# Optimization experiments

Hardware: AMD Instinct MI355X
Metric: run time of the kernel (lower is better)

The kernel has to match this reference:

```python
import jax, jax.numpy as jnp
import numpy as np

MODEL_DIM = 256
HIST = 8
HID = 512
N_NEURONS = 64
IN_DIM = MODEL_DIM * (1 + HIST)  # 2304
BATCH = 32
FMIN, FMAX = 0.5, 40.0
TICK_INTERVAL = 0.1
LN_EPS = 1e-5


def setup_inputs() -> dict:
    key = jax.random.key(0)
    ks = jax.random.split(key, 8)
    def lin(k, shape, fan_in):
        return (jax.random.normal(k, shape, jnp.float32) / np.sqrt(fan_in)).astype(jnp.float32)
    return {
        "input_embedding": jax.random.normal(ks[0], (BATCH, MODEL_DIM), jnp.float32),
        "pre_activations": jax.random.normal(ks[1], (HIST, MODEL_DIM), jnp.float32),
        "Wp": lin(ks[2], (MODEL_DIM, MODEL_DIM), MODEL_DIM),
        "bp": jnp.zeros((MODEL_DIM,), jnp.float32),
        "W1": lin(ks[3], (N_NEURONS, IN_DIM, HID), IN_DIM),
        "b1": jnp.zeros((N_NEURONS, HID), jnp.float32),
        "W2": lin(ks[4], (N_NEURONS, HID, HID), HID),
        "b2": jnp.zeros((N_NEURONS, HID), jnp.float32),
        "W3": lin(ks[5], (N_NEURONS, HID, MODEL_DIM), HID),
        "b3": jnp.zeros((N_NEURONS, MODEL_DIM), jnp.float32),
        "gamma": jnp.ones((N_NEURONS, MODEL_DIM), jnp.float32),
        "beta": jnp.zeros((N_NEURONS, MODEL_DIM), jnp.float32),
        "tick": 7,
    }


def reference(input_embedding, pre_activations, Wp, bp, W1, b1, W2, b2, W3, b3, gamma, beta, tick):
    B = input_embedding.shape[0]
    # input projection, shared history broadcast across batch
    proj = input_embedding @ Wp + bp                               # (B, D)
    hist = jnp.broadcast_to(pre_activations.reshape(-1)[None, :], (B, HIST * MODEL_DIM))
    x = jnp.concatenate([proj, hist], axis=-1)                     # (B, IN_DIM)
    # all neurons' 3-layer MLPs as batched GEMMs (dropout in eval mode = identity)
    h = jax.nn.gelu(jnp.einsum('bi,nih->bnh', x, W1) + b1, approximate=False)
    h = jax.nn.gelu(jnp.einsum('bnh,nhg->bng', h, W2) + b2, approximate=False)
    y = jnp.einsum('bnh,nhd->bnd', h, W3) + b3                     # (B, N, D)
    # per-neuron LayerNorm over last dim
    mu = jnp.mean(y, axis=-1, keepdims=True)
    var = jnp.mean((y - mu) ** 2, axis=-1, keepdims=True)
    y = (y - mu) * jax.lax.rsqrt(var + LN_EPS) * gamma + beta
    # oscillator modulation: log-spaced freq, deterministic phase
    i = jnp.arange(N_NEURONS, dtype=jnp.float32)
    freq = FMIN * (FMAX / FMIN) ** (i / (N_NEURONS - 1))
    phase = jnp.mod(i * 2.3571, 2.0 * np.pi)
    t = tick * TICK_INTERVAL
    mod = 1.0 + 0.5 * jnp.sin(2.0 * np.pi * freq * t + phase)      # (N,)
    return y * mod[None, :, None]                                  # (B, N, D)
```

## Files before the change

### kernel.cpp

```cpp
#include <hip/hip_runtime.h>
#include <hip/hip_bf16.h>

#define MODEL_DIM 256
#define HIST 8
#define HID 512
#define NNEUR 64
#define IN_DIM 2304
#define BATCH 32

__device__ __forceinline__ float geluf(float x) {
    return 0.5f * x * (1.0f + erff(x * 0.70710678118654752440f));
}
__device__ __forceinline__ float f4c(const float4& v, int j) {
    switch (j) { case 0: return v.x; case 1: return v.y; case 2: return v.z; default: return v.w; }
}

__global__ __launch_bounds__(256) void k_build_x(
        const float* __restrict__ emb, const float* __restrict__ pre,
        const float* __restrict__ Wp, const float* __restrict__ bp,
        float* __restrict__ proj) {
    const int b = blockIdx.x;
    const int d = threadIdx.x;

    __shared__ float e[MODEL_DIM];
    e[d] = emb[b * MODEL_DIM + d];
    __syncthreads();

    float acc = bp[d];
    #pragma unroll 4
    for (int k = 0; k < MODEL_DIM; ++k)
        acc = fmaf(e[k], Wp[(size_t)k * MODEL_DIM + d], acc);
    proj[b * MODEL_DIM + d] = acc;
}

__global__ __launch_bounds__(256, 4) void k_layer1(
        const float* __restrict__ pre, const float* __restrict__ proj,
        const float* __restrict__ W1,
        float* __restrict__ ph, float* __restrict__ pp) {
    __shared__ float lds[2048];
    const int bid = blockIdx.x;
    const int t = threadIdx.x;

    if (bid < 512) {
        const int n  = bid >> 3;
        const int ks = bid & 7;
        const int c4 = t & 127;
        const int kh = t >> 7;
        const int k0 = ks * 256;

        float* ps = lds;
        ps[t] = pre[k0 + t];
        __syncthreads();

        const float* W = W1 + (size_t)n * IN_DIM * HID
                            + (size_t)(MODEL_DIM + k0 + kh * 128) * HID + c4 * 4;
        float4 a = make_float4(0.f, 0.f, 0.f, 0.f);
        const float* psk = ps + kh * 128;
        #pragma unroll 8
        for (int kk = 0; kk < 128; ++kk) {
            float4 w = *((const float4*)(W + (size_t)kk * HID));
            float s = psk[kk];
            a.x = fmaf(s, w.x, a.x);
            a.y = fmaf(s, w.y, a.y);
            a.z = fmaf(s, w.z, a.z);
            a.w = fmaf(s, w.w, a.w);
        }
        float4* red = (float4*)(lds + 256);
        if (kh == 1) red[c4] = a;
        __syncthreads();
        if (kh == 0) {
            float4 b4 = red[c4];
            a.x += b4.x; a.y += b4.y; a.z += b4.z; a.w += b4.w;
            *((float4*)(ph + ((size_t)ks * NNEUR + n) * HID + c4 * 4)) = a;
        }
    } else {
        const int pb = bid - 512;
        const int n  = pb >> 3;
        const int ct = (pb >> 2) & 1;
        const int ks = pb & 3;
        const int cg = t & 63;
        const int rg = t >> 6;
        const int col0 = ct * 256 + cg * 4;
        const int row0 = rg * 8;
        const int k0 = ks * 64;

        float (*xs)[64] = (float(*)[64])lds;
        #pragma unroll
        for (int q = 0; q < 2; ++q) {
            int fi  = t + 256 * q;
            int row = fi >> 4;
            int c4  = fi & 15;
            *((float4*)&xs[row][c4 * 4]) =
                *((const float4*)(proj + (size_t)row * MODEL_DIM + k0 + c4 * 4));
        }
        __syncthreads();

        const float* W = W1 + (size_t)n * IN_DIM * HID + (size_t)k0 * HID + col0;

        float acc[8][4];
        #pragma unroll
        for (int i = 0; i < 8; ++i)
            #pragma unroll
            for (int j = 0; j < 4; ++j) acc[i][j] = 0.0f;

        for (int kg = 0; kg < 64; kg += 4) {
            float4 xv[8];
            #pragma unroll
            for (int i = 0; i < 8; ++i)
                xv[i] = *((const float4*)&xs[row0 + i][kg]);
            #pragma unroll
            for (int j = 0; j < 4; ++j) {
                float4 w = *((const float4*)(W + (size_t)(kg + j) * HID));
                #pragma unroll
                for (int i = 0; i < 8; ++i) {
                    float xvv = f4c(xv[i], j);
                    acc[i][0] = fmaf(xvv, w.x, acc[i][0]);
                    acc[i][1] = fmaf(xvv, w.y, acc[i][1]);
                    acc[i][2] = fmaf(xvv, w.z, acc[i][2]);
                    acc[i][3] = fmaf(xvv, w.w, acc[i][3]);
                }
            }
        }
        float* P = pp + (size_t)(ks * NNEUR + n) * BATCH * HID;
        #pragma unroll
        for (int i = 0; i < 8; ++i)
            *((float4*)(P + (size_t)(row0 + i) * HID + col0)) =
                make_float4(acc[i][0], acc[i][1], acc[i][2], acc[i][3]);
    }
}

__global__ __launch_bounds__(256, 4) void k_layer2(
        const float* __restrict__ pp, const float* __restrict__ ph,
        const float* __restrict__ b1,
        const float* __restrict__ W2, float* __restrict__ p2) {
    const int bid = blockIdx.x;
    const int n  = bid >> 4;
    const int ct = (bid >> 3) & 1;
    const int ks = bid & 7;
    const int t  = threadIdx.x;
    const int cg = t & 63;
    const int rg = t >> 6;
    const int col0 = ct * 256 + cg * 4;
    const int row0 = rg * 8;
    const int k0 = ks * 64;

    const size_t slp = (size_t)NNEUR * BATCH * HID;
    const size_t slh = (size_t)NNEUR * HID;

    __shared__ float xs[BATCH][64];
    #pragma unroll
    for (int q = 0; q < 2; ++q) {
        int fi  = t + 256 * q;
        int row = fi >> 4;
        int c4  = fi & 15;
        const float* a = pp + ((size_t)n * BATCH + row) * HID + k0 + c4 * 4;
        float4 s0 = *((const float4*)(a));
        float4 s1 = *((const float4*)(a + slp));
        float4 s2 = *((const float4*)(a + 2 * slp));
        float4 s3 = *((const float4*)(a + 3 * slp));
        const float* h = ph + (size_t)n * HID + k0 + c4 * 4;
        float4 h0 = *((const float4*)(h));
        float4 h1 = *((const float4*)(h + slh));
        float4 h2 = *((const float4*)(h + 2 * slh));
        float4 h3 = *((const float4*)(h + 3 * slh));
        float4 h4 = *((const float4*)(h + 4 * slh));
        float4 h5 = *((const float4*)(h + 5 * slh));
        float4 h6 = *((const float4*)(h + 6 * slh));
        float4 h7 = *((const float4*)(h + 7 * slh));
        float4 bb = *((const float4*)(b1 + (size_t)n * HID + k0 + c4 * 4));
        *((float4*)&xs[row][c4 * 4]) = make_float4(
            geluf(s0.x+s1.x+s2.x+s3.x + h0.x+h1.x+h2.x+h3.x+h4.x+h5.x+h6.x+h7.x + bb.x),
            geluf(s0.y+s1.y+s2.y+s3.y + h0.y+h1.y+h2.y+h3.y+h4.y+h5.y+h6.y+h7.y + bb.y),
            geluf(s0.z+s1.z+s2.z+s3.z + h0.z+h1.z+h2.z+h3.z+h4.z+h5.z+h6.z+h7.z + bb.z),
            geluf(s0.w+s1.w+s2.w+s3.w + h0.w+h1.w+h2.w+h3.w+h4.w+h5.w+h6.w+h7.w + bb.w));
    }
    __syncthreads();

    const float* W = W2 + (size_t)n * HID * HID + (size_t)k0 * HID + col0;

    float acc[8][4];
    #pragma unroll
    for (int i = 0; i < 8; ++i)
        #pragma unroll
        for (int j = 0; j < 4; ++j) acc[i][j] = 0.0f;

    for (int kg = 0; kg < 64; kg += 4) {
        float4 xv[8];
        #pragma unroll
        for (int i = 0; i < 8; ++i)
            xv[i] = *((const float4*)&xs[row0 + i][kg]);
        #pragma unroll
        for (int j = 0; j < 4; ++j) {
            float4 w = *((const float4*)(W + (size_t)(kg + j) * HID));
            #pragma unroll
            for (int i = 0; i < 8; ++i) {
                float xvv = f4c(xv[i], j);
                acc[i][0] = fmaf(xvv, w.x, acc[i][0]);
                acc[i][1] = fmaf(xvv, w.y, acc[i][1]);
                acc[i][2] = fmaf(xvv, w.z, acc[i][2]);
                acc[i][3] = fmaf(xvv, w.w, acc[i][3]);
            }
        }
    }
    float* P = p2 + (size_t)(ks * NNEUR + n) * BATCH * HID;
    #pragma unroll
    for (int i = 0; i < 8; ++i)
        *((float4*)(P + (size_t)(row0 + i) * HID + col0)) =
            make_float4(acc[i][0], acc[i][1], acc[i][2], acc[i][3]);
}

__global__ __launch_bounds__(256, 4) void k_layer3(
        const float* __restrict__ p2, const float* __restrict__ b2,
        const float* __restrict__ W3, float* __restrict__ p3) {
    const int bid = blockIdx.x;
    const int n  = bid >> 4;
    const int ks = bid & 15;
    const int t  = threadIdx.x;
    const int cg = t & 63;
    const int rg = t >> 6;
    const int col0 = cg * 4;
    const int row0 = rg * 8;
    const int k0 = ks * 32;

    const size_t sl = (size_t)NNEUR * BATCH * HID;

    __shared__ float xs[BATCH][32];
    {
        int row = t >> 3;
        int c4  = t & 7;
        const float* a = p2 + ((size_t)n * BATCH + row) * HID + k0 + c4 * 4;
        float4 s0 = *((const float4*)(a));
        float4 s1 = *((const float4*)(a + sl));
        float4 s2 = *((const float4*)(a + 2 * sl));
        float4 s3 = *((const float4*)(a + 3 * sl));
        float4 s4 = *((const float4*)(a + 4 * sl));
        float4 s5 = *((const float4*)(a + 5 * sl));
        float4 s6 = *((const float4*)(a + 6 * sl));
        float4 s7 = *((const float4*)(a + 7 * sl));
        float4 bb = *((const float4*)(b2 + (size_t)n * HID + k0 + c4 * 4));
        *((float4*)&xs[row][c4 * 4]) = make_float4(
            geluf(s0.x+s1.x+s2.x+s3.x+s4.x+s5.x+s6.x+s7.x + bb.x),
            geluf(s0.y+s1.y+s2.y+s3.y+s4.y+s5.y+s6.y+s7.y + bb.y),
            geluf(s0.z+s1.z+s2.z+s3.z+s4.z+s5.z+s6.z+s7.z + bb.z),
            geluf(s0.w+s1.w+s2.w+s3.w+s4.w+s5.w+s6.w+s7.w + bb.w));
    }
    __syncthreads();

    const float* W = W3 + (size_t)n * HID * MODEL_DIM + (size_t)k0 * MODEL_DIM + col0;

    float acc[8][4];
    #pragma unroll
    for (int i = 0; i < 8; ++i)
        #pragma unroll
        for (int j = 0; j < 4; ++j) acc[i][j] = 0.0f;

    for (int kg = 0; kg < 32; kg += 4) {
        float4 xv[8];
        #pragma unroll
        for (int i = 0; i < 8; ++i)
            xv[i] = *((const float4*)&xs[row0 + i][kg]);
        #pragma unroll
        for (int j = 0; j < 4; ++j) {
            float4 w = *((const float4*)(W + (size_t)(kg + j) * MODEL_DIM));
            #pragma unroll
            for (int i = 0; i < 8; ++i) {
                float xvv = f4c(xv[i], j);
                acc[i][0] = fmaf(xvv, w.x, acc[i][0]);
                acc[i][1] = fmaf(xvv, w.y, acc[i][1]);
                acc[i][2] = fmaf(xvv, w.z, acc[i][2]);
                acc[i][3] = fmaf(xvv, w.w, acc[i][3]);
            }
        }
    }
    float* P = p3 + (size_t)(ks * NNEUR + n) * BATCH * MODEL_DIM;
    #pragma unroll
    for (int i = 0; i < 8; ++i)
        *((float4*)(P + (size_t)(row0 + i) * MODEL_DIM + col0)) =
            make_float4(acc[i][0], acc[i][1], acc[i][2], acc[i][3]);
}

__global__ __launch_bounds__(256) void k_final(
        const float* __restrict__ p3, const float* __restrict__ b3,
        const float* __restrict__ gamma, const float* __restrict__ beta,
        const int* __restrict__ tick, float* __restrict__ out) {
    const int n  = blockIdx.x >> 3;
    const int bq = blockIdx.x & 7;
    const int t  = threadIdx.x;
    const int w  = t >> 6;
    const int lane = t & 63;
    const int b  = bq * 4 + w;

    const size_t par0 = (size_t)n * MODEL_DIM;
    const size_t rowoff = ((size_t)n * BATCH + b) * MODEL_DIM;
    const size_t sl = (size_t)NNEUR * BATCH * MODEL_DIM;

    float y[4];
    #pragma unroll
    for (int j = 0; j < 4; ++j) {
        int d = lane + 64 * j;
        float v = b3[par0 + d];
        #pragma unroll
        for (int s = 0; s < 16; ++s)
            v += p3[s * sl + rowoff + d];
        y[j] = v;
    }
    float s = y[0] + y[1] + y[2] + y[3];
    #pragma unroll
    for (int off = 32; off > 0; off >>= 1) s += __shfl_xor(s, off);
    float mu = s * (1.0f / 256.0f);
    float q = 0.0f;
    #pragma unroll
    for (int j = 0; j < 4; ++j) { float d0 = y[j] - mu; q = fmaf(d0, d0, q); }
    #pragma unroll
    for (int off = 32; off > 0; off >>= 1) q += __shfl_xor(q, off);
    float inv = rsqrtf(q * (1.0f / 256.0f) + 1e-5f);

    const double TWO_PI = 6.283185307179586476925287;
    double freq  = 0.5 * pow(80.0, (double)n * (1.0 / 63.0));
    double phase = fmod((double)n * 2.3571, TWO_PI);
    double tt    = (double)(*tick) * 0.1;
    float mod = (float)(1.0 + 0.5 * sin(TWO_PI * freq * tt + phase));

    #pragma unroll
    for (int j = 0; j < 4; ++j) {
        int d = lane + 64 * j;
        float o = (y[j] - mu) * inv * gamma[par0 + d] + beta[par0 + d];
        o *= mod;
        out[((size_t)b * NNEUR + n) * MODEL_DIM + d] = o;
    }
}

extern "C" void kernel_launch(void* const* d_in, const int* in_sizes, int n_in,
                              void* d_out, int out_size, void* d_ws, size_t ws_size,
                              hipStream_t stream) {
    const float* emb  = (const float*)d_in[0];
    const float* pre  = (const float*)d_in[1];
    const float* Wp   = (const float*)d_in[2];
    const float* bp   = (const float*)d_in[3];
    const float* W1   = (const float*)d_in[4];
    const float* b1   = (const float*)d_in[5];
    const float* W2   = (const float*)d_in[6];
    const float* b2   = (const float*)d_in[7];
    const float* W3   = (const float*)d_in[8];
    const float* b3   = (const float*)d_in[9];
    const float* gam  = (const float*)d_in[10];
    const float* bet  = (const float*)d_in[11];
    const int* tick   = (const int*)d_in[12];

    float* ws = (float*)d_ws;
    float* proj = ws;
    float* ph = proj + 8192;
    float* pp = ph + 262144;
    float* p2 = pp + 4194304;
    float* p3 = p2 + 8388608;
    float* out = (float*)d_out;

    k_build_x<<<32,   256, 0, stream>>>(emb, pre, Wp, bp, proj);
    k_layer1 <<<1024, 256, 0, stream>>>(pre, proj, W1, ph, pp);
    k_layer2 <<<1024, 256, 0, stream>>>(pp, ph, b1, W2, p2);
    k_layer3 <<<1024, 256, 0, stream>>>(p2, b2, W3, p3);
    k_final  <<<512,  256, 0, stream>>>(p3, b3, gam, bet, tick, out);
}
```

Measured before the change: 165.2 us.

## Fuse all stages into one cooperative persistent kernel with grid syncs

The five separate launches (projection, layer1, layer2, layer3, final LayerNorm) become one cooperative kernel of 512 blocks, with grid.sync() between stages. Layer1's history and projection parts now run one after the other in each block, and layers 2 and 3 loop two work units per block. The aim is to remove launch gaps and kernel-boundary drains. In exchange it halves parallelism for the layer1 split and serialises the two layer1 halves per block, and grid syncs carry their own cost.

```diff
diff --git a/kernel.cpp b/kernel.cpp
--- a/kernel.cpp
+++ b/kernel.cpp
@@ -1,5 +1,8 @@
 #include <hip/hip_runtime.h>
 #include <hip/hip_bf16.h>
+#include <hip/hip_cooperative_groups.h>
+
+namespace cg = cooperative_groups;
 
 #define MODEL_DIM 256
 #define HIST 8
@@ -15,47 +18,45 @@
     switch (j) { case 0: return v.x; case 1: return v.y; case 2: return v.z; default: return v.w; }
 }
 
-__global__ __launch_bounds__(256) void k_build_x(
+__global__ __launch_bounds__(256, 4) void k_fused(
         const float* __restrict__ emb, const float* __restrict__ pre,
-        const float* __restrict__ Wp, const float* __restrict__ bp,
-        float* __restrict__ proj) {
-    const int b = blockIdx.x;
-    const int d = threadIdx.x;
-
-    __shared__ float e[MODEL_DIM];
-    e[d] = emb[b * MODEL_DIM + d];
-    __syncthreads();
-
-    float acc = bp[d];
-    #pragma unroll 4
-    for (int k = 0; k < MODEL_DIM; ++k)
-        acc = fmaf(e[k], Wp[(size_t)k * MODEL_DIM + d], acc);
-    proj[b * MODEL_DIM + d] = acc;
-}
-
-__global__ __launch_bounds__(256, 4) void k_layer1(
-        const float* __restrict__ pre, const float* __restrict__ proj,
-        const float* __restrict__ W1,
-        float* __restrict__ ph, float* __restrict__ pp) {
+        const float* __restrict__ Wp,  const float* __restrict__ bp,
+        const float* __restrict__ W1,  const float* __restrict__ b1,
+        const float* __restrict__ W2,  const float* __restrict__ b2,
+        const float* __restrict__ W3,  const float* __restrict__ b3,
+        const float* __restrict__ gamma, const float* __restrict__ beta,
+        const int* __restrict__ tick,
+        float* __restrict__ proj, float* __restrict__ ph, float* __restrict__ pp,
+        float* __restrict__ p2,  float* __restrict__ p3, float* __restrict__ out) {
+    cg::grid_group grid = cg::this_grid();
+    const int bid = blockIdx.x;
+    const int t   = threadIdx.x;
     __shared__ float lds[2048];
-    const int bid = blockIdx.x;
-    const int t = threadIdx.x;
-
-    if (bid < 512) {
+
+    if (bid < 32) {
+        const float* e = emb + bid * MODEL_DIM;
+        float acc = bp[t];
+        #pragma unroll 4
+        for (int k = 0; k < MODEL_DIM; ++k)
+            acc = fmaf(e[k], Wp[(size_t)k * MODEL_DIM + t], acc);
+        proj[bid * MODEL_DIM + t] = acc;
+    }
+    grid.sync();
+
+    {
         const int n  = bid >> 3;
         const int ks = bid & 7;
         const int c4 = t & 127;
         const int kh = t >> 7;
         const int k0 = ks * 256;
 
-        float* ps = lds;
-        ps[t] = pre[k0 + t];
+        lds[t] = pre[k0 + t];
         __syncthreads();
 
         const float* W = W1 + (size_t)n * IN_DIM * HID
                             + (size_t)(MODEL_DIM + k0 + kh * 128) * HID + c4 * 4;
         float4 a = make_float4(0.f, 0.f, 0.f, 0.f);
-        const float* psk = ps + kh * 128;
+        const float* psk = lds + kh * 128;
         #pragma unroll 8
         for (int kk = 0; kk < 128; ++kk) {
             float4 w = *((const float4*)(W + (size_t)kk * HID));
@@ -73,11 +74,13 @@
             a.x += b4.x; a.y += b4.y; a.z += b4.z; a.w += b4.w;
             *((float4*)(ph + ((size_t)ks * NNEUR + n) * HID + c4 * 4)) = a;
         }
-    } else {
-        const int pb = bid - 512;
-        const int n  = pb >> 3;
-        const int ct = (pb >> 2) & 1;
-        const int ks = pb & 3;
+        __syncthreads();
+    }
+
+    {
+        const int n  = bid >> 3;
+        const int ct = (bid >> 2) & 1;
+        const int ks = bid & 3;
         const int cg = t & 63;
         const int rg = t >> 6;
         const int col0 = ct * 256 + cg * 4;
@@ -89,9 +92,9 @@
         for (int q = 0; q < 2; ++q) {
             int fi  = t + 256 * q;
             int row = fi >> 4;
-            int c4  = fi & 15;
-            *((float4*)&xs[row][c4 * 4]) =
-                *((const float4*)(proj + (size_t)row * MODEL_DIM + k0 + c4 * 4));
+            int c4v = fi & 15;
+            *((float4*)&xs[row][c4v * 4]) =
+                *((const float4*)(proj + (size_t)row * MODEL_DIM + k0 + c4v * 4));
         }
         __syncthreads();
 
@@ -127,206 +130,200 @@
             *((float4*)(P + (size_t)(row0 + i) * HID + col0)) =
                 make_float4(acc[i][0], acc[i][1], acc[i][2], acc[i][3]);
     }
-}
-
-__global__ __launch_bounds__(256, 4) void k_layer2(
-        const float* __restrict__ pp, const float* __restrict__ ph,
-        const float* __restrict__ b1,
-        const float* __restrict__ W2, float* __restrict__ p2) {
-    const int bid = blockIdx.x;
-    const int n  = bid >> 4;
-    const int ct = (bid >> 3) & 1;
-    const int ks = bid & 7;
-    const int t  = threadIdx.x;
-    const int cg = t & 63;
-    const int rg = t >> 6;
-    const int col0 = ct * 256 + cg * 4;
-    const int row0 = rg * 8;
-    const int k0 = ks * 64;
-
-    const size_t slp = (size_t)NNEUR * BATCH * HID;
-    const size_t slh = (size_t)NNEUR * HID;
-
-    __shared__ float xs[BATCH][64];
-    #pragma unroll
-    for (int q = 0; q < 2; ++q) {
-        int fi  = t + 256 * q;
-        int row = fi >> 4;
-        int c4  = fi & 15;
-        const float* a = pp + ((size_t)n * BATCH + row) * HID + k0 + c4 * 4;
-        float4 s0 = *((const float4*)(a));
-        float4 s1 = *((const float4*)(a + slp));
-        float4 s2 = *((const float4*)(a + 2 * slp));
-        float4 s3 = *((const float4*)(a + 3 * slp));
-        const float* h = ph + (size_t)n * HID + k0 + c4 * 4;
-        float4 h0 = *((const float4*)(h));
-        float4 h1 = *((const float4*)(h + slh));
-        float4 h2 = *((const float4*)(h + 2 * slh));
-        float4 h3 = *((const float4*)(h + 3 * slh));
-        float4 h4 = *((const float4*)(h + 4 * slh));
-        float4 h5 = *((const float4*)(h + 5 * slh));
-        float4 h6 = *((const float4*)(h + 6 * slh));
-        float4 h7 = *((const float4*)(h + 7 * slh));
-        float4 bb = *((const float4*)(b1 + (size_t)n * HID + k0 + c4 * 4));
-        *((float4*)&xs[row][c4 * 4]) = make_float4(
-            geluf(s0.x+s1.x+s2.x+s3.x + h0.x+h1.x+h2.x+h3.x+h4.x+h5.x+h6.x+h7.x + bb.x),
-            geluf(s0.y+s1.y+s2.y+s3.y + h0.y+h1.y+h2.y+h3.y+h4.y+h5.y+h6.y+h7.y + bb.y),
-            geluf(s0.z+s1.z+s2.z+s3.z + h0.z+h1.z+h2.z+h3.z+h4.z+h5.z+h6.z+h7.z + bb.z),
-            geluf(s0.w+s1.w+s2.w+s3.w + h0.w+h1.w+h2.w+h3.w+h4.w+h5.w+h6.w+h7.w + bb.w));
-    }
-    __syncthreads();
-
-    const float* W = W2 + (size_t)n * HID * HID + (size_t)k0 * HID + col0;
-
-    float acc[8][4];
-    #pragma unroll
-    for (int i = 0; i < 8; ++i)
-        #pragma unroll
-        for (int j = 0; j < 4; ++j) acc[i][j] = 0.0f;
-
-    for (int kg = 0; kg < 64; kg += 4) {
-        float4 xv[8];
-        #pragma unroll
-        for (int i = 0; i < 8; ++i)
-            xv[i] = *((const float4*)&xs[row0 + i][kg]);
+    grid.sync();
+
+    #pragma unroll 1
+    for (int u = bid; u < 1024; u += 512) {
+        const int n  = u >> 4;
+        const int ct = (u >> 3) & 1;
+        const int ks = u & 7;
+        const int cg = t & 63;
+        const int rg = t >> 6;
+        const int col0 = ct * 256 + cg * 4;
+        const int row0 = rg * 8;
+        const int k0 = ks * 64;
+
+        const size_t slp = (size_t)NNEUR * BATCH * HID;
+        const size_t slh = (size_t)NNEUR * HID;
+
+        float (*xs)[64] = (float(*)[64])lds;
+        __syncthreads();
+        #pragma unroll
+        for (int q = 0; q < 2; ++q) {
+            int fi  = t + 256 * q;
+            int row = fi >> 4;
+            int c4v = fi & 15;
+            const float* a = pp + ((size_t)n * BATCH + row) * HID + k0 + c4v * 4;
+            float4 s0 = *((const float4*)(a));
+            float4 s1 = *((const float4*)(a + slp));
+            float4 s2 = *((const float4*)(a + 2 * slp));
+            float4 s3 = *((const float4*)(a + 3 * slp));
+            const float* h = ph + (size_t)n * HID + k0 + c4v * 4;
+            float4 h0 = *((const float4*)(h));
+            float4 h1 = *((const float4*)(h + slh));
+            float4 h2 = *((const float4*)(h + 2 * slh));
+            float4 h3 = *((const float4*)(h + 3 * slh));
+            float4 h4 = *((const float4*)(h + 4 * slh));
+            float4 h5 = *((const float4*)(h + 5 * slh));
+            float4 h6 = *((const float4*)(h + 6 * slh));
+            float4 h7 = *((const float4*)(h + 7 * slh));
+            float4 bb = *((const float4*)(b1 + (size_t)n * HID + k0 + c4v * 4));
+            *((float4*)&xs[row][c4v * 4]) = make_float4(
+                geluf(s0.x+s1.x+s2.x+s3.x + h0.x+h1.x+h2.x+h3.x+h4.x+h5.x+h6.x+h7.x + bb.x),
+                geluf(s0.y+s1.y+s2.y+s3.y + h0.y+h1.y+h2.y+h3.y+h4.y+h5.y+h6.y+h7.y + bb.y),
+                geluf(s0.z+s1.z+s2.z+s3.z + h0.z+h1.z+h2.z+h3.z+h4.z+h5.z+h6.z+h7.z + bb.z),
+                geluf(s0.w+s1.w+s2.w+s3.w + h0.w+h1.w+h2.w+h3.w+h4.w+h5.w+h6.w+h7.w + bb.w));
+        }
+        __syncthreads();
+
+        const float* W = W2 + (size_t)n * HID * HID + (size_t)k0 * HID + col0;
+
+        float acc[8][4];
+        #pragma unroll
+        for (int i = 0; i < 8; ++i)
+            #pragma unroll
+            for (int j = 0; j < 4; ++j) acc[i][j] = 0.0f;
+
+        for (int kg = 0; kg < 64; kg += 4) {
+            float4 xv[8];
+            #pragma unroll
+            for (int i = 0; i < 8; ++i)
+                xv[i] = *((const float4*)&xs[row0 + i][kg]);
+            #pragma unroll
+            for (int j = 0; j < 4; ++j) {
+                float4 w = *((const float4*)(W + (size_t)(kg + j) * HID));
+                #pragma unroll
+                for (int i = 0; i < 8; ++i) {
+                    float xvv = f4c(xv[i], j);
+                    acc[i][0] = fmaf(xvv, w.x, acc[i][0]);
+                    acc[i][1] = fmaf(xvv, w.y, acc[i][1]);
+                    acc[i][2] = fmaf(xvv, w.z, acc[i][2]);
+                    acc[i][3] = fmaf(xvv, w.w, acc[i][3]);
+                }
+            }
+        }
+        float* P = p2 + (size_t)(ks * NNEUR + n) * BATCH * HID;
+        #pragma unroll
+        for (int i = 0; i < 8; ++i)
+            *((float4*)(P + (size_t)(row0 + i) * HID + col0)) =
+                make_float4(acc[i][0], acc[i][1], acc[i][2], acc[i][3]);
+    }
+    grid.sync();
+
+    #pragma unroll 1
+    for (int u = bid; u < 1024; u += 512) {
+        const int n  = u >> 4;
+        const int ks = u & 15;
+        const int cg = t & 63;
+        const int rg = t >> 6;
+        const int col0 = cg * 4;
+        const int row0 = rg * 8;
+        const int k0 = ks * 32;
+
+        const size_t sl = (size_t)NNEUR * BATCH * HID;
+
+        float (*xs)[32] = (float(*)[32])lds;
+        __syncthreads();
+        {
+            int row = t >> 3;
+            int c4v = t & 7;
+            const float* a = p2 + ((size_t)n * BATCH + row) * HID + k0 + c4v * 4;
+            float4 s0 = *((const float4*)(a));
+            float4 s1 = *((const float4*)(a + sl));
+            float4 s2 = *((const float4*)(a + 2 * sl));
+            float4 s3 = *((const float4*)(a + 3 * sl));
+            float4 s4 = *((const float4*)(a + 4 * sl));
+            float4 s5 = *((const float4*)(a + 5 * sl));
+            float4 s6 = *((const float4*)(a + 6 * sl));
+            float4 s7 = *((const float4*)(a + 7 * sl));
+            float4 bb = *((const float4*)(b2 + (size_t)n * HID + k0 + c4v * 4));
+            *((float4*)&xs[row][c4v * 4]) = make_float4(
+                geluf(s0.x+s1.x+s2.x+s3.x+s4.x+s5.x+s6.x+s7.x + bb.x),
+                geluf(s0.y+s1.y+s2.y+s3.y+s4.y+s5.y+s6.y+s7.y + bb.y),
+                geluf(s0.z+s1.z+s2.z+s3.z+s4.z+s5.z+s6.z+s7.z + bb.z),
+                geluf(s0.w+s1.w+s2.w+s3.w+s4.w+s5.w+s6.w+s7.w + bb.w));
+        }
+        __syncthreads();
+
+        const float* W = W3 + (size_t)n * HID * MODEL_DIM + (size_t)k0 * MODEL_DIM + col0;
+
+        float acc[8][4];
+        #pragma unroll
+        for (int i = 0; i < 8; ++i)
+            #pragma unroll
+            for (int j = 0; j < 4; ++j) acc[i][j] = 0.0f;
+
+        for (int kg = 0; kg < 32; kg += 4) {
+            float4 xv[8];
+            #pragma unroll
+            for (int i = 0; i < 8; ++i)
+                xv[i] = *((const float4*)&xs[row0 + i][kg]);
+            #pragma unroll
+            for (int j = 0; j < 4; ++j) {
+                float4 w = *((const float4*)(W + (size_t)(kg + j) * MODEL_DIM));
+                #pragma unroll
+                for (int i = 0; i < 8; ++i) {
+                    float xvv = f4c(xv[i], j);
+                    acc[i][0] = fmaf(xvv, w.x, acc[i][0]);
+                    acc[i][1] = fmaf(xvv, w.y, acc[i][1]);
+                    acc[i][2] = fmaf(xvv, w.z, acc[i][2]);
+                    acc[i][3] = fmaf(xvv, w.w, acc[i][3]);
+                }
+            }
+        }
+        float* P = p3 + (size_t)(ks * NNEUR + n) * BATCH * MODEL_DIM;
+        #pragma unroll
+        for (int i = 0; i < 8; ++i)
+            *((float4*)(P + (size_t)(row0 + i) * MODEL_DIM + col0)) =
+                make_float4(acc[i][0], acc[i][1], acc[i][2], acc[i][3]);
+    }
+    grid.sync();
+
+    {
+        const int n  = bid >> 3;
+        const int bq = bid & 7;
+        const int w  = t >> 6;
+        const int lane = t & 63;
+        const int b  = bq * 4 + w;
+
+        const size_t par0 = (size_t)n * MODEL_DIM;
+        const size_t rowoff = ((size_t)n * BATCH + b) * MODEL_DIM;
+        const size_t sl = (size_t)NNEUR * BATCH * MODEL_DIM;
+
+        float y[4];
         #pragma unroll
         for (int j = 0; j < 4; ++j) {
-            float4 w = *((const float4*)(W + (size_t)(kg + j) * HID));
-            #pragma unroll
-            for (int i = 0; i < 8; ++i) {
-                float xvv = f4c(xv[i], j);
-                acc[i][0] = fmaf(xvv, w.x, acc[i][0]);
-                acc[i][1] = fmaf(xvv, w.y, acc[i][1]);
-                acc[i][2] = fmaf(xvv, w.z, acc[i][2]);
-                acc[i][3] = fmaf(xvv, w.w, acc[i][3]);
-            }
-        }
-    }
-    float* P = p2 + (size_t)(ks * NNEUR + n) * BATCH * HID;
-    #pragma unroll
-    for (int i = 0; i < 8; ++i)
-        *((float4*)(P + (size_t)(row0 + i) * HID + col0)) =
-            make_float4(acc[i][0], acc[i][1], acc[i][2], acc[i][3]);
-}
-
-__global__ __launch_bounds__(256, 4) void k_layer3(
-        const float* __restrict__ p2, const float* __restrict__ b2,
-        const float* __restrict__ W3, float* __restrict__ p3) {
-    const int bid = blockIdx.x;
-    const int n  = bid >> 4;
-    const int ks = bid & 15;
-    const int t  = threadIdx.x;
-    const int cg = t & 63;
-    const int rg = t >> 6;
-    const int col0 = cg * 4;
-    const int row0 = rg * 8;
-    const int k0 = ks * 32;
-
-    const size_t sl = (size_t)NNEUR * BATCH * HID;
-
-    __shared__ float xs[BATCH][32];
-    {
-        int row = t >> 3;
-        int c4  = t & 7;
-        const float* a = p2 + ((size_t)n * BATCH + row) * HID + k0 + c4 * 4;
-        float4 s0 = *((const float4*)(a));
-        float4 s1 = *((const float4*)(a + sl));
-        float4 s2 = *((const float4*)(a + 2 * sl));
-        float4 s3 = *((const float4*)(a + 3 * sl));
-        float4 s4 = *((const float4*)(a + 4 * sl));
-        float4 s5 = *((const float4*)(a + 5 * sl));
-        float4 s6 = *((const float4*)(a + 6 * sl));
-        float4 s7 = *((const float4*)(a + 7 * sl));
-        float4 bb = *((const float4*)(b2 + (size_t)n * HID + k0 + c4 * 4));
-        *((float4*)&xs[row][c4 * 4]) = make_float4(
-            geluf(s0.x+s1.x+s2.x+s3.x+s4.x+s5.x+s6.x+s7.x + bb.x),
-            geluf(s0.y+s1.y+s2.y+s3.y+s4.y+s5.y+s6.y+s7.y + bb.y),
-            geluf(s0.z+s1.z+s2.z+s3.z+s4.z+s5.z+s6.z+s7.z + bb.z),
-            geluf(s0.w+s1.w+s2.w+s3.w+s4.w+s5.w+s6.w+s7.w + bb.w));
-    }
-    __syncthreads();
-
-    const float* W = W3 + (size_t)n * HID * MODEL_DIM + (size_t)k0 * MODEL_DIM + col0;
-
-    float acc[8][4];
-    #pragma unroll
-    for (int i = 0; i < 8; ++i)
-        #pragma unroll
-        for (int j = 0; j < 4; ++j) acc[i][j] = 0.0f;
-
-    for (int kg = 0; kg < 32; kg += 4) {
-        float4 xv[8];
-        #pragma unroll
-        for (int i = 0; i < 8; ++i)
-            xv[i] = *((const float4*)&xs[row0 + i][kg]);
+            int d = lane + 64 * j;
+            float v = b3[par0 + d];
+            #pragma unroll
+            for (int s = 0; s < 16; ++s)
+                v += p3[s * sl + rowoff + d];
+            y[j] = v;
+        }
+        float s = y[0] + y[1] + y[2] + y[3];
+        #pragma unroll
+        for (int off = 32; off > 0; off >>= 1) s += __shfl_xor(s, off);
+        float mu = s * (1.0f / 256.0f);
+        float q = 0.0f;
+        #pragma unroll
+        for (int j = 0; j < 4; ++j) { float d0 = y[j] - mu; q = fmaf(d0, d0, q); }
+        #pragma unroll
+        for (int off = 32; off > 0; off >>= 1) q += __shfl_xor(q, off);
+        float inv = rsqrtf(q * (1.0f / 256.0f) + 1e-5f);
+
+        const double TWO_PI = 6.283185307179586476925287;
+        double freq  = 0.5 * pow(80.0, (double)n * (1.0 / 63.0));
+        double phase = fmod((double)n * 2.3571, TWO_PI);
+        double tt    = (double)(*tick) * 0.1;
+        float mod = (float)(1.0 + 0.5 * sin(TWO_PI * freq * tt + phase));
+
         #pragma unroll
         for (int j = 0; j < 4; ++j) {
-            float4 w = *((const float4*)(W + (size_t)(kg + j) * MODEL_DIM));
-            #pragma unroll
-            for (int i = 0; i < 8; ++i) {
-                float xvv = f4c(xv[i], j);
-                acc[i][0] = fmaf(xvv, w.x, acc[i][0]);
-                acc[i][1] = fmaf(xvv, w.y, acc[i][1]);
-                acc[i][2] = fmaf(xvv, w.z, acc[i][2]);
-                acc[i][3] = fmaf(xvv, w.w, acc[i][3]);
-            }
-        }
-    }
-    float* P = p3 + (size_t)(ks * NNEUR + n) * BATCH * MODEL_DIM;
-    #pragma unroll
-    for (int i = 0; i < 8; ++i)
-        *((float4*)(P + (size_t)(row0 + i) * MODEL_DIM + col0)) =
-            make_float4(acc[i][0], acc[i][1], acc[i][2], acc[i][3]);
-}
-
-__global__ __launch_bounds__(256) void k_final(
-        const float* __restrict__ p3, const float* __restrict__ b3,
-        const float* __restrict__ gamma, const float* __restrict__ beta,
-        const int* __restrict__ tick, float* __restrict__ out) {
-    const int n  = blockIdx.x >> 3;
-    const int bq = blockIdx.x & 7;
-    const int t  = threadIdx.x;
-    const int w  = t >> 6;
-    const int lane = t & 63;
-    const int b  = bq * 4 + w;
-
-    const size_t par0 = (size_t)n * MODEL_DIM;
-    const size_t rowoff = ((size_t)n * BATCH + b) * MODEL_DIM;
-    const size_t sl = (size_t)NNEUR * BATCH * MODEL_DIM;
-
-    float y[4];
-    #pragma unroll
-    for (int j = 0; j < 4; ++j) {
-        int d = lane + 64 * j;
-        float v = b3[par0 + d];
-        #pragma unroll
-        for (int s = 0; s < 16; ++s)
-            v += p3[s * sl + rowoff + d];
-        y[j] = v;
-    }
-    float s = y[0] + y[1] + y[2] + y[3];
-    #pragma unroll
-    for (int off = 32; off > 0; off >>= 1) s += __shfl_xor(s, off);
-    float mu = s * (1.0f / 256.0f);
-    float q = 0.0f;
-    #pragma unroll
-    for (int j = 0; j < 4; ++j) { float d0 = y[j] - mu; q = fmaf(d0, d0, q); }
-    #pragma unroll
-    for (int off = 32; off > 0; off >>= 1) q += __shfl_xor(q, off);
-    float inv = rsqrtf(q * (1.0f / 256.0f) + 1e-5f);
-
-    const double TWO_PI = 6.283185307179586476925287;
-    double freq  = 0.5 * pow(80.0, (double)n * (1.0 / 63.0));
-    double phase = fmod((double)n * 2.3571, TWO_PI);
-    double tt    = (double)(*tick) * 0.1;
-    float mod = (float)(1.0 + 0.5 * sin(TWO_PI * freq * tt + phase));
-
-    #pragma unroll
-    for (int j = 0; j < 4; ++j) {
-        int d = lane + 64 * j;
-        float o = (y[j] - mu) * inv * gamma[par0 + d] + beta[par0 + d];
-        o *= mod;
-        out[((size_t)b * NNEUR + n) * MODEL_DIM + d] = o;
+            int d = lane + 64 * j;
+            float o = (y[j] - mu) * inv * gamma[par0 + d] + beta[par0 + d];
+            o *= mod;
+            out[((size_t)b * NNEUR + n) * MODEL_DIM + d] = o;
+        }
     }
 }
 
@@ -355,9 +352,13 @@
     float* p3 = p2 + 8388608;
     float* out = (float*)d_out;
 
-    k_build_x<<<32,   256, 0, stream>>>(emb, pre, Wp, bp, proj);
-    k_layer1 <<<1024, 256, 0, stream>>>(pre, proj, W1, ph, pp);
-    k_layer2 <<<1024, 256, 0, stream>>>(pp, ph, b1, W2, p2);
-    k_layer3 <<<1024, 256, 0, stream>>>(p2, b2, W3, p3);
-    k_final  <<<512,  256, 0, stream>>>(p3, b3, gam, bet, tick, out);
+    void* args[] = {
+        (void*)&emb, (void*)&pre, (void*)&Wp, (void*)&bp,
+        (void*)&W1, (void*)&b1, (void*)&W2, (void*)&b2,
+        (void*)&W3, (void*)&b3, (void*)&gam, (void*)&bet,
+        (void*)&tick, (void*)&proj, (void*)&ph, (void*)&pp,
+        (void*)&p2, (void*)&p3, (void*)&out
+    };
+    hipLaunchCooperativeKernel((const void*)k_fused, dim3(512), dim3(256),
+                               args, 0, stream);
 }
```

Measured after the change: 387.4 us. 135% more time.

## Split layer-1 into separate history GEMV and projection GEMM kernels

Applied to the files above, without the earlier changes.

The fused layer-1 kernel, which mixed history GEMV blocks and projection GEMM blocks, becomes two kernels. The history kernel now uses 1024 blocks with 16 K-slices of 128 rows, 8 columns per thread and a 4-way LDS reduction, which gives more parallelism for streaming the large W1 history slab. Layer 2 now sums 16 history partials instead of 8, and the workspace for them is doubled. The cost is an extra launch, more partial-sum traffic, and losing the concurrency of the fused launch.

```diff
diff --git a/kernel.cpp b/kernel.cpp
--- a/kernel.cpp
+++ b/kernel.cpp
@@ -33,110 +33,62 @@
     proj[b * MODEL_DIM + d] = acc;
 }
 
-__global__ __launch_bounds__(256, 4) void k_layer1(
-        const float* __restrict__ pre, const float* __restrict__ proj,
-        const float* __restrict__ W1,
-        float* __restrict__ ph, float* __restrict__ pp) {
-    __shared__ float lds[2048];
+__global__ __launch_bounds__(256, 4) void k_hist(
+        const float* __restrict__ pre, const float* __restrict__ W1,
+        float* __restrict__ ph) {
+    const int n  = blockIdx.x >> 4;
+    const int ks = blockIdx.x & 15;
+    const int t  = threadIdx.x;
+    const int w  = t >> 6;
+    const int l  = t & 63;
+    const int k0 = ks * 128;
+
+    __shared__ float ps[128];
+    __shared__ float red[4][512];
+    if (t < 128) ps[t] = pre[k0 + t];
+    __syncthreads();
+
+    const float* W = W1 + (size_t)n * IN_DIM * HID
+                        + (size_t)(MODEL_DIM + k0 + w * 32) * HID + l * 8;
+    const float* pw = ps + w * 32;
+
+    float4 a0 = make_float4(0.f, 0.f, 0.f, 0.f);
+    float4 a1 = make_float4(0.f, 0.f, 0.f, 0.f);
+    #pragma unroll 4
+    for (int kk = 0; kk < 32; ++kk) {
+        float4 w0 = *((const float4*)(W + (size_t)kk * HID));
+        float4 w1 = *((const float4*)(W + (size_t)kk * HID + 4));
+        float s = pw[kk];
+        a0.x = fmaf(s, w0.x, a0.x); a0.y = fmaf(s, w0.y, a0.y);
+        a0.z = fmaf(s, w0.z, a0.z); a0.w = fmaf(s, w0.w, a0.w);
+        a1.x = fmaf(s, w1.x, a1.x); a1.y = fmaf(s, w1.y, a1.y);
+        a1.z = fmaf(s, w1.z, a1.z); a1.w = fmaf(s, w1.w, a1.w);
+    }
+    *((float4*)&red[w][l * 8])     = a0;
+    *((float4*)&red[w][l * 8 + 4]) = a1;
+    __syncthreads();
+
+    if (t < 128) {
+        const int c = t * 4;
+        float4 r0 = *((const float4*)&red[0][c]);
+        float4 r1 = *((const float4*)&red[1][c]);
+        float4 r2 = *((const float4*)&red[2][c]);
+        float4 r3 = *((const float4*)&red[3][c]);
+        float4 o = make_float4(r0.x + r1.x + r2.x + r3.x,
+                               r0.y + r1.y + r2.y + r3.y,
+                               r0.z + r1.z + r2.z + r3.z,
+                               r0.w + r1.w + r2.w + r3.w);
+        *((float4*)(ph + ((size_t)ks * NNEUR + n) * HID + c)) = o;
+    }
+}
+
+__global__ __launch_bounds__(256, 4) void k_proj(
+        const float* __restrict__ proj, const float* __restrict__ W1,
+        float* __restrict__ pp) {
     const int bid = blockIdx.x;
-    const int t = threadIdx.x;
-
-    if (bid < 512) {
-        const int n  = bid >> 3;
-        const int ks = bid & 7;
-        const int c4 = t & 127;
-        const int kh = t >> 7;
-        const int k0 = ks * 256;
-
-        float* ps = lds;
-        ps[t] = pre[k0 + t];
-        __syncthreads();
-
-        const float* W = W1 + (size_t)n * IN_DIM * HID
-                            + (size_t)(MODEL_DIM + k0 + kh * 128) * HID + c4 * 4;
-        float4 a = make_float4(0.f, 0.f, 0.f, 0.f);
-        const float* psk = ps + kh * 128;
-        #pragma unroll 8
-        for (int kk = 0; kk < 128; ++kk) {
-            float4 w = *((const float4*)(W + (size_t)kk * HID));
-            float s = psk[kk];
-            a.x = fmaf(s, w.x, a.x);
-            a.y = fmaf(s, w.y, a.y);
-            a.z = fmaf(s, w.z, a.z);
-            a.w = fmaf(s, w.w, a.w);
-        }
-        float4* red = (float4*)(lds + 256);
-        if (kh == 1) red[c4] = a;
-        __syncthreads();
-        if (kh == 0) {
-            float4 b4 = red[c4];
-            a.x += b4.x; a.y += b4.y; a.z += b4.z; a.w += b4.w;
-            *((float4*)(ph + ((size_t)ks * NNEUR + n) * HID + c4 * 4)) = a;
-        }
-    } else {
-        const int pb = bid - 512;
-        const int n  = pb >> 3;
-        const int ct = (pb >> 2) & 1;
-        const int ks = pb & 3;
-        const int cg = t & 63;
-        const int rg = t >> 6;
-        const int col0 = ct * 256 + cg * 4;
-        const int row0 = rg * 8;
-        const int k0 = ks * 64;
-
-        float (*xs)[64] = (float(*)[64])lds;
-        #pragma unroll
-        for (int q = 0; q < 2; ++q) {
-            int fi  = t + 256 * q;
-            int row = fi >> 4;
-            int c4  = fi & 15;
-            *((float4*)&xs[row][c4 * 4]) =
-                *((const float4*)(proj + (size_t)row * MODEL_DIM + k0 + c4 * 4));
-        }
-        __syncthreads();
-
-        const float* W = W1 + (size_t)n * IN_DIM * HID + (size_t)k0 * HID + col0;
-
-        float acc[8][4];
-        #pragma unroll
-        for (int i = 0; i < 8; ++i)
-            #pragma unroll
-            for (int j = 0; j < 4; ++j) acc[i][j] = 0.0f;
-
-        for (int kg = 0; kg < 64; kg += 4) {
-            float4 xv[8];
-            #pragma unroll
-            for (int i = 0; i < 8; ++i)
-                xv[i] = *((const float4*)&xs[row0 + i][kg]);
-            #pragma unroll
-            for (int j = 0; j < 4; ++j) {
-                float4 w = *((const float4*)(W + (size_t)(kg + j) * HID));
-                #pragma unroll
-                for (int i = 0; i < 8; ++i) {
-                    float xvv = f4c(xv[i], j);
-                    acc[i][0] = fmaf(xvv, w.x, acc[i][0]);
-                    acc[i][1] = fmaf(xvv, w.y, acc[i][1]);
-                    acc[i][2] = fmaf(xvv, w.z, acc[i][2]);
-                    acc[i][3] = fmaf(xvv, w.w, acc[i][3]);
-                }
-            }
-        }
-        float* P = pp + (size_t)(ks * NNEUR + n) * BATCH * HID;
-        #pragma unroll
-        for (int i = 0; i < 8; ++i)
-            *((float4*)(P + (size_t)(row0 + i) * HID + col0)) =
-                make_float4(acc[i][0], acc[i][1], acc[i][2], acc[i][3]);
-    }
-}
-
-__global__ __launch_bounds__(256, 4) void k_layer2(
-        const float* __restrict__ pp, const float* __restrict__ ph,
-        const float* __restrict__ b1,
-        const float* __restrict__ W2, float* __restrict__ p2) {
-    const int bid = blockIdx.x;
-    const int n  = bid >> 4;
-    const int ct = (bid >> 3) & 1;
-    const int ks = bid & 7;
+    const int n  = bid >> 3;
+    const int ct = (bid >> 2) & 1;
+    const int ks = bid & 3;
     const int t  = threadIdx.x;
     const int cg = t & 63;
     const int rg = t >> 6;
@@ -144,39 +96,18 @@
     const int row0 = rg * 8;
     const int k0 = ks * 64;
 
-    const size_t slp = (size_t)NNEUR * BATCH * HID;
-    const size_t slh = (size_t)NNEUR * HID;
-
     __shared__ float xs[BATCH][64];
     #pragma unroll
     for (int q = 0; q < 2; ++q) {
         int fi  = t + 256 * q;
         int row = fi >> 4;
-        int c4  = fi & 15;
-        const float* a = pp + ((size_t)n * BATCH + row) * HID + k0 + c4 * 4;
-        float4 s0 = *((const float4*)(a));
-        float4 s1 = *((const float4*)(a + slp));
-        float4 s2 = *((const float4*)(a + 2 * slp));
-        float4 s3 = *((const float4*)(a + 3 * slp));
-        const float* h = ph + (size_t)n * HID + k0 + c4 * 4;
-        float4 h0 = *((const float4*)(h));
-        float4 h1 = *((const float4*)(h + slh));
-        float4 h2 = *((const float4*)(h + 2 * slh));
-        float4 h3 = *((const float4*)(h + 3 * slh));
-        float4 h4 = *((const float4*)(h + 4 * slh));
-        float4 h5 = *((const float4*)(h + 5 * slh));
-        float4 h6 = *((const float4*)(h + 6 * slh));
-        float4 h7 = *((const float4*)(h + 7 * slh));
-        float4 bb = *((const float4*)(b1 + (size_t)n * HID + k0 + c4 * 4));
-        *((float4*)&xs[row][c4 * 4]) = make_float4(
-            geluf(s0.x+s1.x+s2.x+s3.x + h0.x+h1.x+h2.x+h3.x+h4.x+h5.x+h6.x+h7.x + bb.x),
-            geluf(s0.y+s1.y+s2.y+s3.y + h0.y+h1.y+h2.y+h3.y+h4.y+h5.y+h6.y+h7.y + bb.y),
-            geluf(s0.z+s1.z+s2.z+s3.z + h0.z+h1.z+h2.z+h3.z+h4.z+h5.z+h6.z+h7.z + bb.z),
-            geluf(s0.w+s1.w+s2.w+s3.w + h0.w+h1.w+h2.w+h3.w+h4.w+h5.w+h6.w+h7.w + bb.w));
-    }
-    __syncthreads();
-
-    const float* W = W2 + (size_t)n * HID * HID + (size_t)k0 * HID + col0;
+        int c4v = fi & 15;
+        *((float4*)&xs[row][c4v * 4]) =
+            *((const float4*)(proj + (size_t)row * MODEL_DIM + k0 + c4v * 4));
+    }
+    __syncthreads();
+
+    const float* W = W1 + (size_t)n * IN_DIM * HID + (size_t)k0 * HID + col0;
 
     float acc[8][4];
     #pragma unroll
@@ -202,6 +133,84 @@
             }
         }
     }
+    float* P = pp + (size_t)(ks * NNEUR + n) * BATCH * HID;
+    #pragma unroll
+    for (int i = 0; i < 8; ++i)
+        *((float4*)(P + (size_t)(row0 + i) * HID + col0)) =
+            make_float4(acc[i][0], acc[i][1], acc[i][2], acc[i][3]);
+}
+
+__global__ __launch_bounds__(256, 4) void k_layer2(
+        const float* __restrict__ pp, const float* __restrict__ ph,
+        const float* __restrict__ b1,
+        const float* __restrict__ W2, float* __restrict__ p2) {
+    const int bid = blockIdx.x;
+    const int n  = bid >> 4;
+    const int ct = (bid >> 3) & 1;
+    const int ks = bid & 7;
+    const int t  = threadIdx.x;
+    const int cg = t & 63;
+    const int rg = t >> 6;
+    const int col0 = ct * 256 + cg * 4;
+    const int row0 = rg * 8;
+    const int k0 = ks * 64;
+
+    const size_t slp = (size_t)NNEUR * BATCH * HID;
+    const size_t slh = (size_t)NNEUR * HID;
+
+    __shared__ float xs[BATCH][64];
+    #pragma unroll
+    for (int q = 0; q < 2; ++q) {
+        int fi  = t + 256 * q;
+        int row = fi >> 4;
+        int c4v = fi & 15;
+        const float* a = pp + ((size_t)n * BATCH + row) * HID + k0 + c4v * 4;
+        float4 s0 = *((const float4*)(a));
+        float4 s1 = *((const float4*)(a + slp));
+        float4 s2 = *((const float4*)(a + 2 * slp));
+        float4 s3 = *((const float4*)(a + 3 * slp));
+        float4 hs = make_float4(0.f, 0.f, 0.f, 0.f);
+        const float* h = ph + (size_t)n * HID + k0 + c4v * 4;
+        #pragma unroll
+        for (int s5 = 0; s5 < 16; ++s5) {
+            float4 hv = *((const float4*)(h + (size_t)s5 * slh));
+            hs.x += hv.x; hs.y += hv.y; hs.z += hv.z; hs.w += hv.w;
+        }
+        float4 bb = *((const float4*)(b1 + (size_t)n * HID + k0 + c4v * 4));
+        *((float4*)&xs[row][c4v * 4]) = make_float4(
+            geluf(s0.x + s1.x + s2.x + s3.x + hs.x + bb.x),
+            geluf(s0.y + s1.y + s2.y + s3.y + hs.y + bb.y),
+            geluf(s0.z + s1.z + s2.z + s3.z + hs.z + bb.z),
+            geluf(s0.w + s1.w + s2.w + s3.w + hs.w + bb.w));
+    }
+    __syncthreads();
+
+    const float* W = W2 + (size_t)n * HID * HID + (size_t)k0 * HID + col0;
+
+    float acc[8][4];
+    #pragma unroll
+    for (int i = 0; i < 8; ++i)
+        #pragma unroll
+        for (int j = 0; j < 4; ++j) acc[i][j] = 0.0f;
+
+    for (int kg = 0; kg < 64; kg += 4) {
+        float4 xv[8];
+        #pragma unroll
+        for (int i = 0; i < 8; ++i)
+            xv[i] = *((const float4*)&xs[row0 + i][kg]);
+        #pragma unroll
+        for (int j = 0; j < 4; ++j) {
+            float4 w = *((const float4*)(W + (size_t)(kg + j) * HID));
+            #pragma unroll
+            for (int i = 0; i < 8; ++i) {
+                float xvv = f4c(xv[i], j);
+                acc[i][0] = fmaf(xvv, w.x, acc[i][0]);
+                acc[i][1] = fmaf(xvv, w.y, acc[i][1]);
+                acc[i][2] = fmaf(xvv, w.z, acc[i][2]);
+                acc[i][3] = fmaf(xvv, w.w, acc[i][3]);
+            }
+        }
+    }
     float* P = p2 + (size_t)(ks * NNEUR + n) * BATCH * HID;
     #pragma unroll
     for (int i = 0; i < 8; ++i)
@@ -227,8 +236,8 @@
     __shared__ float xs[BATCH][32];
     {
         int row = t >> 3;
-        int c4  = t & 7;
-        const float* a = p2 + ((size_t)n * BATCH + row) * HID + k0 + c4 * 4;
+        int c4v = t & 7;
+        const float* a = p2 + ((size_t)n * BATCH + row) * HID + k0 + c4v * 4;
         float4 s0 = *((const float4*)(a));
         float4 s1 = *((const float4*)(a + sl));
         float4 s2 = *((const float4*)(a + 2 * sl));
@@ -237,8 +246,8 @@
         float4 s5 = *((const float4*)(a + 5 * sl));
         float4 s6 = *((const float4*)(a + 6 * sl));
         float4 s7 = *((const float4*)(a + 7 * sl));
-        float4 bb = *((const float4*)(b2 + (size_t)n * HID + k0 + c4 * 4));
-        *((float4*)&xs[row][c4 * 4]) = make_float4(
+        float4 bb = *((const float4*)(b2 + (size_t)n * HID + k0 + c4v * 4));
+        *((float4*)&xs[row][c4v * 4]) = make_float4(
             geluf(s0.x+s1.x+s2.x+s3.x+s4.x+s5.x+s6.x+s7.x + bb.x),
             geluf(s0.y+s1.y+s2.y+s3.y+s4.y+s5.y+s6.y+s7.y + bb.y),
             geluf(s0.z+s1.z+s2.z+s3.z+s4.z+s5.z+s6.z+s7.z + bb.z),
@@ -350,13 +359,14 @@
     float* ws = (float*)d_ws;
     float* proj = ws;
     float* ph = proj + 8192;
-    float* pp = ph + 262144;
+    float* pp = ph + 524288;
     float* p2 = pp + 4194304;
     float* p3 = p2 + 8388608;
     float* out = (float*)d_out;
 
     k_build_x<<<32,   256, 0, stream>>>(emb, pre, Wp, bp, proj);
-    k_layer1 <<<1024, 256, 0, stream>>>(pre, proj, W1, ph, pp);
+    k_hist   <<<1024, 256, 0, stream>>>(pre, W1, ph);
+    k_proj   <<<512,  256, 0, stream>>>(proj, W1, pp);
     k_layer2 <<<1024, 256, 0, stream>>>(pp, ph, b1, W2, p2);
     k_layer3 <<<1024, 256, 0, stream>>>(p2, b2, W3, p3);
     k_final  <<<512,  256, 0, stream>>>(p3, b3, gam, bet, tick, out);
```

New measurement: 175.3 us. 1.06x slower.
